# Performance work log

Measured on AMD Instinct MI355X. Metric: run time of the kernel, lower is better.

Reference implementation:

```python
import jax, jax.numpy as jnp
import numpy as np

N = 200000   # active voxels
C = 128      # in_channels == out_channels -> identity downsample
K = 27       # 3x3x3 kernel offsets
EPS = 1e-5


def setup_inputs() -> dict:
    key = jax.random.key(0)
    ks = jax.random.split(key, 4)
    x = jax.random.normal(ks[0], (N, C), jnp.float32)
    nbr = jax.random.randint(ks[1], (N, K), 0, N, jnp.int32)
    W1 = jax.random.normal(ks[2], (K, C, C), jnp.float32) * 0.05
    W2 = jax.random.normal(ks[3], (K, C, C), jnp.float32) * 0.05
    g1 = jnp.ones((C,), jnp.float32); b1 = jnp.zeros((C,), jnp.float32)
    g2 = jnp.ones((C,), jnp.float32); b2 = jnp.zeros((C,), jnp.float32)
    return {"x": x, "nbr": nbr, "W1": W1, "g1": g1, "b1": b1,
            "W2": W2, "g2": g2, "b2": b2}


def _sparse_conv(x, nbr, W):
    # gather-matmul-scatter sparse conv: out[i] = sum_k W[k]^T x[nbr[i,k]]
    # scan over the K=27 kernel offsets to avoid materializing [N,K,C].
    def body(acc, kn):
        Wk, nk = kn                               # [C,C], [N]
        return acc + jnp.take(x, nk, axis=0) @ Wk, None
    acc0 = jnp.zeros((x.shape[0], W.shape[2]), x.dtype)
    out, _ = jax.lax.scan(body, acc0, (W, nbr.T))
    return out


def _bn(x, g, b):
    # training-mode batch norm over the point dimension
    m = jnp.mean(x, axis=0)
    v = jnp.var(x, axis=0)
    return (x - m) * jax.lax.rsqrt(v + EPS) * g + b


def reference(x, nbr, W1, g1, b1, W2, g2, b2):
    out = jax.nn.relu(_bn(_sparse_conv(x, nbr, W1), g1, b1))
    out = _bn(_sparse_conv(out, nbr, W2), g2, b2)
    # downsample is identity (in_channels == out_channels, stride == 1)
    return jax.nn.relu(out + x)
```

## Files before the change

### kernel.cpp

```cpp
#include <hip/hip_runtime.h>
#include <hip/hip_bf16.h>
#include <stdint.h>

#define C_DIM 128
#define K_DIM 27

typedef __attribute__((ext_vector_type(8))) short short8;
typedef __attribute__((ext_vector_type(4))) float f32x4;
typedef __attribute__((ext_vector_type(4))) unsigned short ushort4v;

#define VMCNT8() asm volatile("s_waitcnt vmcnt(8)" ::: "memory")
#define VMCNT6() asm volatile("s_waitcnt vmcnt(6)" ::: "memory")
#define VMCNT4() asm volatile("s_waitcnt vmcnt(4)" ::: "memory")
#define VMCNT0() asm volatile("s_waitcnt vmcnt(0)" ::: "memory")
#define LGKM0() asm volatile("s_waitcnt lgkmcnt(0)" ::: "memory")
#define BAR() __builtin_amdgcn_s_barrier()

__device__ __forceinline__ unsigned short f2bf(float f) {
  unsigned int u = __builtin_bit_cast(unsigned int, f);
  u += 0x7fffu + ((u >> 16) & 1u);
  return (unsigned short)(u >> 16);
}
__device__ __forceinline__ float bf2f(unsigned short h) {
  unsigned int u = ((unsigned int)h) << 16;
  return __builtin_bit_cast(float, u);
}

__device__ __forceinline__ void async_copy16(const void* gsrc, void* ldst) {
  __builtin_amdgcn_global_load_lds(
      (const __attribute__((address_space(1))) unsigned int*)gsrc,
      (__attribute__((address_space(3))) unsigned int*)ldst, 16, 0, 0);
}

__global__ __launch_bounds__(256) void prep_kernel(
    const float* __restrict__ W1, const float* __restrict__ W2,
    unsigned short* __restrict__ Wt1, unsigned short* __restrict__ Wt2,
    float* __restrict__ stats, int stats_n) {
  int idx = blockIdx.x * 256 + threadIdx.x;
  const int total = K_DIM * C_DIM * C_DIM;
  if (idx < total) {
    int cq = idx & 31;
    int co = (idx >> 5) & 127;
    int q  = (idx >> 12) & 3;
    int k  = idx >> 14;
    int ci = q * 32 + cq;
    int src = (k * C_DIM + ci) * C_DIM + co;
    Wt1[idx] = f2bf(W1[src]);
    Wt2[idx] = f2bf(W2[src]);
  }
  if (idx < stats_n) stats[idx] = 0.f;
}

__global__ __launch_bounds__(256) void cvt_x_kernel(
    const float* __restrict__ x, unsigned short* __restrict__ xb, int total4) {
  int i = blockIdx.x * 256 + threadIdx.x;
  if (i >= total4) return;
  f32x4 v = ((const f32x4*)x)[i];
  ushort4v u;
#pragma unroll
  for (int j = 0; j < 4; ++j) u[j] = f2bf(v[j]);
  ((ushort4v*)xb)[i] = u;
}

template<int OUT_IS_F32>
__global__ __launch_bounds__(256, 3) void conv_kernel(
    const unsigned short* __restrict__ xb, const int* __restrict__ nbr,
    const unsigned short* __restrict__ Wt, void* __restrict__ out_v,
    float* __restrict__ stats, int N) {
  extern __shared__ __align__(16) char smem[];
  unsigned short* Abuf = (unsigned short*)smem;
  int* idx_lds = (int*)(smem + 32768);
  float* s_sum = (float*)(smem + 32768 + 13824);
  float* s_ssum = s_sum + C_DIM;

  const int tid = threadIdx.x;
  const int wave = tid >> 6, lane = tid & 63;
  const int lr = lane & 15, lg = lane >> 4;
  const int rg = wave >> 1, cg = wave & 1;
  const int row0 = blockIdx.x * 128;

  if (tid < C_DIM) { s_sum[tid] = 0.f; s_ssum[tid] = 0.f; }

  for (int i = tid; i < 128 * K_DIM; i += 256) {
    int r = i / K_DIM;
    int k = i - r * K_DIM;
    int rr = row0 + r; if (rr >= N) rr = N - 1;
    idx_lds[i] = nbr[(size_t)rr * K_DIM + k];
  }
  __syncthreads();

  const int srow = lane >> 2;
  const int ssw = ((lane & 3) ^ (srow & 3)) << 3;
  const int gr0 = wave * 32 + srow;
  const int gr1 = gr0 + 16;

  auto stage = [&](int a0i, int a1i, int q, int buf) {
    unsigned short* dst = Abuf + buf * 4096 + wave * 1024;
    async_copy16(xb + (size_t)a0i * C_DIM + q * 32 + ssw, dst);
    async_copy16(xb + (size_t)a1i * C_DIM + q * 32 + ssw, dst + 512);
  };

  const unsigned short* wbase = Wt + (size_t)(cg * 64 + lr) * 32 + lg * 8;
  short8 wE[4], wO[4];
  auto wload = [&](short8 (&w)[4], int p) {
    const unsigned short* wp = wbase + (size_t)p * 4096;
#pragma unroll
    for (int ct = 0; ct < 4; ++ct)
      w[ct] = *(const short8*)(wp + ct * 512);
  };

  f32x4 acc[4][4] = {};
  const unsigned short* abase =
      Abuf + (rg * 64 + lr) * 32 + ((lg ^ (lr & 3)) << 3);

  auto compute = [&](const unsigned short* ab, const short8 (&w)[4]) {
    short8 a[4];
#pragma unroll
    for (int rt = 0; rt < 4; ++rt)
      a[rt] = *(const short8*)(ab + rt * 512);
    __builtin_amdgcn_s_setprio(1);
#pragma unroll
    for (int rt = 0; rt < 4; ++rt)
#pragma unroll
      for (int ct = 0; ct < 4; ++ct)
        acc[rt][ct] = __builtin_amdgcn_mfma_f32_16x16x32_bf16(a[rt], w[ct], acc[rt][ct], 0, 0, 0);
    __builtin_amdgcn_s_setprio(0);
  };

  int gA = idx_lds[gr0 * K_DIM];
  int gB = idx_lds[gr1 * K_DIM];
  stage(gA, gB, 0, 0);
  wload(wE, 0);
  stage(gA, gB, 1, 1);
  stage(gA, gB, 2, 2);
  VMCNT8();
  BAR();

  for (int base = 0; base < 104; base += 4) {
    const int k1 = (base >> 2) + 1;
    int hA, hB;
    wload(wO, base + 1);
    stage(gA, gB, 3, 3);
    hA = idx_lds[gr0 * K_DIM + k1];
    hB = idx_lds[gr1 * K_DIM + k1];
    VMCNT8();
    compute(abase, wE);
    LGKM0(); BAR();
    wload(wE, base + 2);
    stage(hA, hB, 0, 0);
    VMCNT8();
    compute(abase + 4096, wO);
    LGKM0(); BAR();
    wload(wO, base + 3);
    stage(hA, hB, 1, 1);
    VMCNT8();
    compute(abase + 8192, wE);
    LGKM0(); BAR();
    wload(wE, base + 4);
    stage(hA, hB, 2, 2);
    VMCNT8();
    compute(abase + 12288, wO);
    LGKM0(); BAR();
    gA = hA; gB = hB;
  }

  wload(wO, 105);
  stage(gA, gB, 3, 3);
  VMCNT8();
  compute(abase, wE);
  LGKM0(); BAR();
  wload(wE, 106);
  VMCNT6();
  compute(abase + 4096, wO);
  LGKM0(); BAR();
  wload(wO, 107);
  VMCNT4();
  compute(abase + 8192, wE);
  LGKM0(); BAR();
  VMCNT0();
  compute(abase + 12288, wO);

  float ps[4] = {0.f, 0.f, 0.f, 0.f}, pss[4] = {0.f, 0.f, 0.f, 0.f};
#pragma unroll
  for (int rt = 0; rt < 4; ++rt) {
#pragma unroll
    for (int j = 0; j < 4; ++j) {
      int grow = row0 + rg * 64 + rt * 16 + lg * 4 + j;
      bool ok = grow < N;
#pragma unroll
      for (int ct = 0; ct < 4; ++ct) {
        float v = acc[rt][ct][j];
        if (ok) {
          int col = cg * 64 + ct * 16 + lr;
          if (OUT_IS_F32)
            ((float*)out_v)[(size_t)grow * C_DIM + col] = v;
          else
            ((unsigned short*)out_v)[(size_t)grow * C_DIM + col] = f2bf(v);
          ps[ct] += v;
          pss[ct] += v * v;
        }
      }
    }
  }
#pragma unroll
  for (int ct = 0; ct < 4; ++ct) {
    ps[ct]  += __shfl_xor(ps[ct], 16, 64);
    ps[ct]  += __shfl_xor(ps[ct], 32, 64);
    pss[ct] += __shfl_xor(pss[ct], 16, 64);
    pss[ct] += __shfl_xor(pss[ct], 32, 64);
    if (lg == 0) {
      int col = cg * 64 + ct * 16 + lr;
      atomicAdd(&s_sum[col], ps[ct]);
      atomicAdd(&s_ssum[col], pss[ct]);
    }
  }
  __syncthreads();
  if (tid < C_DIM) {
    atomicAdd(&stats[tid], s_sum[tid]);
    atomicAdd(&stats[C_DIM + tid], s_ssum[tid]);
  }
}

__global__ void finalize_kernel(const float* __restrict__ stats,
                                const float* __restrict__ g,
                                const float* __restrict__ b,
                                float* __restrict__ sshift, float invN) {
  int c = threadIdx.x;
  float mean = stats[c] * invN;
  float var = stats[128 + c] * invN - mean * mean;
  float sc = g[c] * rsqrtf(var + 1e-5f);
  sshift[c] = sc;
  sshift[128 + c] = b[c] - mean * sc;
}

__global__ __launch_bounds__(256) void apply_kernel(
    unsigned short* __restrict__ y, const float* __restrict__ ss, int total8) {
  int i = blockIdx.x * 256 + threadIdx.x;
  if (i >= total8) return;
  int cb = (i * 8) & 127;
  short8 u = ((short8*)y)[i];
#pragma unroll
  for (int j = 0; j < 8; ++j) {
    float f = bf2f((unsigned short)u[j]) * ss[cb + j] + ss[128 + cb + j];
    u[j] = (short)f2bf(fmaxf(f, 0.f));
  }
  ((short8*)y)[i] = u;
}

__global__ __launch_bounds__(256) void final_kernel(
    float* __restrict__ y2, const float* __restrict__ x,
    const float* __restrict__ ss, int total4) {
  int i = blockIdx.x * 256 + threadIdx.x;
  if (i >= total4) return;
  int cb = (i * 4) & 127;
  f32x4 v = ((const f32x4*)y2)[i];
  f32x4 xv = ((const f32x4*)x)[i];
#pragma unroll
  for (int j = 0; j < 4; ++j)
    v[j] = fmaxf(v[j] * ss[cb + j] + ss[128 + cb + j] + xv[j], 0.f);
  ((f32x4*)y2)[i] = v;
}

extern "C" void kernel_launch(void* const* d_in, const int* in_sizes, int n_in,
                              void* d_out, int out_size, void* d_ws, size_t ws_size,
                              hipStream_t stream) {
  const float* x  = (const float*)d_in[0];
  const int* nbr  = (const int*)d_in[1];
  const float* W1 = (const float*)d_in[2];
  const float* g1 = (const float*)d_in[3];
  const float* b1 = (const float*)d_in[4];
  const float* W2 = (const float*)d_in[5];
  const float* g2 = (const float*)d_in[6];
  const float* b2 = (const float*)d_in[7];
  float* out = (float*)d_out;

  const int N = in_sizes[0] / C_DIM;
  const int totalW = K_DIM * C_DIM * C_DIM;
  const int SMEM_BYTES = 32768 + 13824 + 1024;

  char* ws = (char*)d_ws;
  size_t off = 0;
  auto alloc = [&](size_t bytes) {
    void* p = ws + off;
    off = (off + bytes + 255) & ~(size_t)255;
    return p;
  };
  unsigned short* Wt1 = (unsigned short*)alloc((size_t)totalW * 2);
  unsigned short* Wt2 = (unsigned short*)alloc((size_t)totalW * 2);
  float* stats = (float*)alloc(512 * 4);
  float* ss1   = (float*)alloc(256 * 4);
  float* ss2   = (float*)alloc(256 * 4);
  unsigned short* y1 = (unsigned short*)alloc((size_t)N * C_DIM * 2);
  unsigned short* xb_ws = (unsigned short*)alloc((size_t)N * C_DIM * 2);
  unsigned short* xb = (off <= ws_size) ? xb_ws : (unsigned short*)d_out;

  const int nblk = (N + 127) / 128;
  const float invN = 1.0f / (float)N;

  prep_kernel<<<(totalW + 255) / 256, 256, 0, stream>>>(W1, W2, Wt1, Wt2, stats, 512);

  {
    int t4 = N * C_DIM / 4;
    cvt_x_kernel<<<(t4 + 255) / 256, 256, 0, stream>>>(x, xb, t4);
  }

  conv_kernel<0><<<nblk, 256, SMEM_BYTES, stream>>>(xb, nbr, Wt1, y1, stats, N);
  finalize_kernel<<<1, 128, 0, stream>>>(stats, g1, b1, ss1, invN);

  {
    int t8 = N * C_DIM / 8;
    apply_kernel<<<(t8 + 255) / 256, 256, 0, stream>>>(y1, ss1, t8);
  }

  conv_kernel<1><<<nblk, 256, SMEM_BYTES, stream>>>(y1, nbr, Wt2, out, stats + 256, N);
  finalize_kernel<<<1, 128, 0, stream>>>(stats + 256, g2, b2, ss2, invN);

  {
    int t4 = N * C_DIM / 4;
    final_kernel<<<(t4 + 255) / 256, 256, 0, stream>>>(out, x, ss2, t4);
  }
}
```

Baseline: 656.4 us.

## Deepen weight prefetch to two stages and change LDS swizzle pattern

Result: no change. 652.0 us (-0.7%).

```diff
diff --git a/kernel.cpp b/kernel.cpp
--- a/kernel.cpp
+++ b/kernel.cpp
@@ -9,10 +9,11 @@
 typedef __attribute__((ext_vector_type(4))) float f32x4;
 typedef __attribute__((ext_vector_type(4))) unsigned short ushort4v;
 
-#define VMCNT8() asm volatile("s_waitcnt vmcnt(8)" ::: "memory")
-#define VMCNT6() asm volatile("s_waitcnt vmcnt(6)" ::: "memory")
-#define VMCNT4() asm volatile("s_waitcnt vmcnt(4)" ::: "memory")
-#define VMCNT0() asm volatile("s_waitcnt vmcnt(0)" ::: "memory")
+#define FENCE() asm volatile("" ::: "memory")
+#define VMCNT12() asm volatile("s_waitcnt vmcnt(12)" ::: "memory")
+#define VMCNT10() asm volatile("s_waitcnt vmcnt(10)" ::: "memory")
+#define VMCNT4()  asm volatile("s_waitcnt vmcnt(4)" ::: "memory")
+#define VMCNT0()  asm volatile("s_waitcnt vmcnt(0)" ::: "memory")
 #define LGKM0() asm volatile("s_waitcnt lgkmcnt(0)" ::: "memory")
 #define BAR() __builtin_amdgcn_s_barrier()
 
@@ -89,9 +90,8 @@
   }
   __syncthreads();
 
-  const int srow = lane >> 2;
-  const int ssw = ((lane & 3) ^ (srow & 3)) << 3;
-  const int gr0 = wave * 32 + srow;
+  const int ssw = ((lane & 3) ^ ((lane >> 3) & 3)) << 3;
+  const int gr0 = wave * 32 + (lane >> 2);
   const int gr1 = gr0 + 16;
 
   auto stage = [&](int a0i, int a1i, int q, int buf) {
@@ -101,84 +101,88 @@
   };
 
   const unsigned short* wbase = Wt + (size_t)(cg * 64 + lr) * 32 + lg * 8;
-  short8 wE[4], wO[4];
-  auto wload = [&](short8 (&w)[4], int p) {
-    const unsigned short* wp = wbase + (size_t)p * 4096;
-#pragma unroll
-    for (int ct = 0; ct < 4; ++ct)
-      w[ct] = *(const short8*)(wp + ct * 512);
-  };
+  short8 w0[4], w1[4], w2[4], w3[4];
+#define WLOAD(W, P)                                                      \
+  do {                                                                   \
+    const unsigned short* wp_ = wbase + (size_t)(P) * 4096;              \
+    _Pragma("unroll")                                                    \
+    for (int ct = 0; ct < 4; ++ct) W[ct] = *(const short8*)(wp_ + ct * 512); \
+  } while (0)
 
   f32x4 acc[4][4] = {};
   const unsigned short* abase =
-      Abuf + (rg * 64 + lr) * 32 + ((lg ^ (lr & 3)) << 3);
-
-  auto compute = [&](const unsigned short* ab, const short8 (&w)[4]) {
-    short8 a[4];
-#pragma unroll
-    for (int rt = 0; rt < 4; ++rt)
-      a[rt] = *(const short8*)(ab + rt * 512);
-    __builtin_amdgcn_s_setprio(1);
-#pragma unroll
-    for (int rt = 0; rt < 4; ++rt)
-#pragma unroll
-      for (int ct = 0; ct < 4; ++ct)
-        acc[rt][ct] = __builtin_amdgcn_mfma_f32_16x16x32_bf16(a[rt], w[ct], acc[rt][ct], 0, 0, 0);
-    __builtin_amdgcn_s_setprio(0);
-  };
+      Abuf + (rg * 64 + lr) * 32 + ((lg ^ ((lr >> 1) & 3)) << 3);
+
+#define COMPUTE(BUFOFS, W)                                               \
+  do {                                                                   \
+    short8 a_[4];                                                        \
+    _Pragma("unroll")                                                    \
+    for (int rt = 0; rt < 4; ++rt)                                       \
+      a_[rt] = *(const short8*)(abase + (BUFOFS) + rt * 512);            \
+    __builtin_amdgcn_s_setprio(1);                                       \
+    _Pragma("unroll")                                                    \
+    for (int rt = 0; rt < 4; ++rt)                                       \
+      _Pragma("unroll")                                                  \
+      for (int ct = 0; ct < 4; ++ct)                                     \
+        acc[rt][ct] = __builtin_amdgcn_mfma_f32_16x16x32_bf16(           \
+            a_[rt], W[ct], acc[rt][ct], 0, 0, 0);                        \
+    __builtin_amdgcn_s_setprio(0);                                       \
+  } while (0)
 
   int gA = idx_lds[gr0 * K_DIM];
   int gB = idx_lds[gr1 * K_DIM];
-  stage(gA, gB, 0, 0);
-  wload(wE, 0);
-  stage(gA, gB, 1, 1);
-  stage(gA, gB, 2, 2);
-  VMCNT8();
+  stage(gA, gB, 0, 0); FENCE();
+  stage(gA, gB, 1, 1); FENCE();
+  WLOAD(w0, 0); FENCE();
+  stage(gA, gB, 2, 2); FENCE();
+  WLOAD(w1, 1); FENCE();
+  VMCNT12();
   BAR();
 
   for (int base = 0; base < 104; base += 4) {
     const int k1 = (base >> 2) + 1;
     int hA, hB;
-    wload(wO, base + 1);
-    stage(gA, gB, 3, 3);
+    stage(gA, gB, 3, 3); FENCE();
+    WLOAD(w2, base + 2); FENCE();
     hA = idx_lds[gr0 * K_DIM + k1];
     hB = idx_lds[gr1 * K_DIM + k1];
-    VMCNT8();
-    compute(abase, wE);
+    VMCNT12();
+    COMPUTE(0, w0);
     LGKM0(); BAR();
-    wload(wE, base + 2);
-    stage(hA, hB, 0, 0);
-    VMCNT8();
-    compute(abase + 4096, wO);
+    stage(hA, hB, 0, 0); FENCE();
+    WLOAD(w3, base + 3); FENCE();
+    VMCNT12();
+    COMPUTE(4096, w1);
     LGKM0(); BAR();
-    wload(wO, base + 3);
-    stage(hA, hB, 1, 1);
-    VMCNT8();
-    compute(abase + 8192, wE);
+    stage(hA, hB, 1, 1); FENCE();
+    WLOAD(w0, base + 4); FENCE();
+    VMCNT12();
+    COMPUTE(8192, w2);
     LGKM0(); BAR();
-    wload(wE, base + 4);
-    stage(hA, hB, 2, 2);
-    VMCNT8();
-    compute(abase + 12288, wO);
+    stage(hA, hB, 2, 2); FENCE();
+    WLOAD(w1, base + 5); FENCE();
+    VMCNT12();
+    COMPUTE(12288, w3);
     LGKM0(); BAR();
     gA = hA; gB = hB;
   }
 
-  wload(wO, 105);
-  stage(gA, gB, 3, 3);
-  VMCNT8();
-  compute(abase, wE);
+  stage(gA, gB, 3, 3); FENCE();
+  WLOAD(w2, 106); FENCE();
+  VMCNT12();
+  COMPUTE(0, w0);
   LGKM0(); BAR();
-  wload(wE, 106);
-  VMCNT6();
-  compute(abase + 4096, wO);
+  WLOAD(w3, 107); FENCE();
+  VMCNT10();
+  COMPUTE(4096, w1);
   LGKM0(); BAR();
-  wload(wO, 107);
   VMCNT4();
-  compute(abase + 8192, wE);
+  COMPUTE(8192, w2);
   LGKM0(); BAR();
   VMCNT0();
-  compute(abase + 12288, wO);
+  COMPUTE(12288, w3);
+#undef WLOAD
+#undef COMPUTE
 
   float ps[4] = {0.f, 0.f, 0.f, 0.f}, pss[4] = {0.f, 0.f, 0.f, 0.f};
 #pragma unroll
```

## Stage weights in LDS, double block rows, transpose neighbor indices

Applied to the files above, without the earlier changes.

New measurement: 600.1 us. 1.09x faster.

```diff
diff --git a/kernel.cpp b/kernel.cpp
--- a/kernel.cpp
+++ b/kernel.cpp
@@ -9,9 +9,8 @@
 typedef __attribute__((ext_vector_type(4))) float f32x4;
 typedef __attribute__((ext_vector_type(4))) unsigned short ushort4v;
 
-#define VMCNT8() asm volatile("s_waitcnt vmcnt(8)" ::: "memory")
-#define VMCNT6() asm volatile("s_waitcnt vmcnt(6)" ::: "memory")
-#define VMCNT4() asm volatile("s_waitcnt vmcnt(4)" ::: "memory")
+#define VMCNT5() asm volatile("s_waitcnt vmcnt(5)" ::: "memory")
+#define VMCNT3() asm volatile("s_waitcnt vmcnt(3)" ::: "memory")
 #define VMCNT0() asm volatile("s_waitcnt vmcnt(0)" ::: "memory")
 #define LGKM0() asm volatile("s_waitcnt lgkmcnt(0)" ::: "memory")
 #define BAR() __builtin_amdgcn_s_barrier()
@@ -39,16 +38,33 @@
   int idx = blockIdx.x * 256 + threadIdx.x;
   const int total = K_DIM * C_DIM * C_DIM;
   if (idx < total) {
-    int cq = idx & 31;
+    int e = idx & 7;
+    int gpos = (idx >> 3) & 3;
     int co = (idx >> 5) & 127;
-    int q  = (idx >> 12) & 3;
-    int k  = idx >> 14;
-    int ci = q * 32 + cq;
+    int p = idx >> 12;
+    int k = p >> 2, q = p & 3;
+    int ci = q * 32 + ((gpos ^ ((co >> 1) & 3)) << 3) + e;
     int src = (k * C_DIM + ci) * C_DIM + co;
     Wt1[idx] = f2bf(W1[src]);
     Wt2[idx] = f2bf(W2[src]);
   }
   if (idx < stats_n) stats[idx] = 0.f;
+}
+
+__global__ __launch_bounds__(256) void tr_kernel(
+    const int* __restrict__ nbr, int* __restrict__ nbrT, int N) {
+  __shared__ int t[64 * K_DIM];
+  const int row0 = blockIdx.x * 64;
+  for (int i = threadIdx.x; i < 64 * K_DIM; i += 256) {
+    int r = i / K_DIM, kk = i - r * K_DIM;
+    int rr = row0 + r;
+    t[kk * 64 + r] = (rr < N) ? nbr[(size_t)rr * K_DIM + kk] : 0;
+  }
+  __syncthreads();
+  for (int j = threadIdx.x; j < K_DIM * 64; j += 256) {
+    int kk = j >> 6, r = j & 63;
+    if (row0 + r < N) nbrT[(size_t)kk * N + row0 + r] = t[j];
+  }
 }
 
 __global__ __launch_bounds__(256) void cvt_x_kernel(
@@ -63,122 +79,107 @@
 }
 
 template<int OUT_IS_F32>
-__global__ __launch_bounds__(256, 3) void conv_kernel(
-    const unsigned short* __restrict__ xb, const int* __restrict__ nbr,
+__global__ __launch_bounds__(512, 4) void conv_kernel(
+    const unsigned short* __restrict__ xb, const int* __restrict__ nbrT,
     const unsigned short* __restrict__ Wt, void* __restrict__ out_v,
     float* __restrict__ stats, int N) {
   extern __shared__ __align__(16) char smem[];
   unsigned short* Abuf = (unsigned short*)smem;
-  int* idx_lds = (int*)(smem + 32768);
-  float* s_sum = (float*)(smem + 32768 + 13824);
+  unsigned short* Wbuf = (unsigned short*)(smem + 49152);
+  float* s_sum = (float*)(smem + 73728);
   float* s_ssum = s_sum + C_DIM;
 
   const int tid = threadIdx.x;
   const int wave = tid >> 6, lane = tid & 63;
   const int lr = lane & 15, lg = lane >> 4;
   const int rg = wave >> 1, cg = wave & 1;
-  const int row0 = blockIdx.x * 128;
+  const int row0 = blockIdx.x * 256;
 
   if (tid < C_DIM) { s_sum[tid] = 0.f; s_ssum[tid] = 0.f; }
 
-  for (int i = tid; i < 128 * K_DIM; i += 256) {
-    int r = i / K_DIM;
-    int k = i - r * K_DIM;
-    int rr = row0 + r; if (rr >= N) rr = N - 1;
-    idx_lds[i] = nbr[(size_t)rr * K_DIM + k];
-  }
-  __syncthreads();
-
   const int srow = lane >> 2;
-  const int ssw = ((lane & 3) ^ (srow & 3)) << 3;
-  const int gr0 = wave * 32 + srow;
-  const int gr1 = gr0 + 16;
-
-  auto stage = [&](int a0i, int a1i, int q, int buf) {
-    unsigned short* dst = Abuf + buf * 4096 + wave * 1024;
-    async_copy16(xb + (size_t)a0i * C_DIM + q * 32 + ssw, dst);
-    async_copy16(xb + (size_t)a1i * C_DIM + q * 32 + ssw, dst + 512);
+  const int ssw = ((lane & 3) ^ ((srow >> 1) & 3)) << 3;
+  int rA = row0 + wave * 32 + srow;      if (rA >= N) rA = N - 1;
+  int rB = row0 + wave * 32 + 16 + srow; if (rB >= N) rB = N - 1;
+
+  auto stage_a = [&](int giA, int giB, int q, int aofs) {
+    unsigned short* dst = Abuf + aofs + wave * 1024;
+    async_copy16(xb + (size_t)giA * C_DIM + q * 32 + ssw, dst);
+    async_copy16(xb + (size_t)giB * C_DIM + q * 32 + ssw, dst + 512);
   };
-
-  const unsigned short* wbase = Wt + (size_t)(cg * 64 + lr) * 32 + lg * 8;
-  short8 wE[4], wO[4];
-  auto wload = [&](short8 (&w)[4], int p) {
-    const unsigned short* wp = wbase + (size_t)p * 4096;
+  auto stage_w = [&](const unsigned short* wsrc, int wofs) {
+    async_copy16(wsrc + wave * 512 + lane * 8, Wbuf + wofs + wave * 512);
+  };
+
+  f32x4 acc[4][4] = {};
+  const int swzr = (lg ^ ((lr >> 1) & 3)) << 3;
+  const int aro = (rg * 64 + lr) * 32 + swzr;
+  const int wro = (cg * 64 + lr) * 32 + swzr;
+
+  auto compute = [&](int cAo, int cWo) {
+    short8 a_[4], b_[4];
+#pragma unroll
+    for (int rt = 0; rt < 4; ++rt)
+      a_[rt] = *(const short8*)(Abuf + cAo + aro + rt * 512);
 #pragma unroll
     for (int ct = 0; ct < 4; ++ct)
-      w[ct] = *(const short8*)(wp + ct * 512);
-  };
-
-  f32x4 acc[4][4] = {};
-  const unsigned short* abase =
-      Abuf + (rg * 64 + lr) * 32 + ((lg ^ (lr & 3)) << 3);
-
-  auto compute = [&](const unsigned short* ab, const short8 (&w)[4]) {
-    short8 a[4];
+      b_[ct] = *(const short8*)(Wbuf + cWo + wro + ct * 512);
+    __builtin_amdgcn_s_setprio(1);
 #pragma unroll
     for (int rt = 0; rt < 4; ++rt)
-      a[rt] = *(const short8*)(ab + rt * 512);
-    __builtin_amdgcn_s_setprio(1);
-#pragma unroll
-    for (int rt = 0; rt < 4; ++rt)
 #pragma unroll
       for (int ct = 0; ct < 4; ++ct)
-        acc[rt][ct] = __builtin_amdgcn_mfma_f32_16x16x32_bf16(a[rt], w[ct], acc[rt][ct], 0, 0, 0);
+        acc[rt][ct] = __builtin_amdgcn_mfma_f32_16x16x32_bf16(
+            a_[rt], b_[ct], acc[rt][ct], 0, 0, 0);
     __builtin_amdgcn_s_setprio(0);
   };
 
-  int gA = idx_lds[gr0 * K_DIM];
-  int gB = idx_lds[gr1 * K_DIM];
-  stage(gA, gB, 0, 0);
-  wload(wE, 0);
-  stage(gA, gB, 1, 1);
-  stage(gA, gB, 2, 2);
-  VMCNT8();
+  int giA = nbrT[rA];
+  int giB = nbrT[rB];
+  stage_a(giA, giB, 0, 0);     stage_w(Wt, 0);
+  stage_a(giA, giB, 1, 8192);  stage_w(Wt + 4096, 4096);
+  VMCNT3();
   BAR();
 
-  for (int base = 0; base < 104; base += 4) {
-    const int k1 = (base >> 2) + 1;
-    int hA, hB;
-    wload(wO, base + 1);
-    stage(gA, gB, 3, 3);
-    hA = idx_lds[gr0 * K_DIM + k1];
-    hB = idx_lds[gr1 * K_DIM + k1];
-    VMCNT8();
-    compute(abase, wE);
-    LGKM0(); BAR();
-    wload(wE, base + 2);
-    stage(hA, hB, 0, 0);
-    VMCNT8();
-    compute(abase + 4096, wO);
-    LGKM0(); BAR();
-    wload(wO, base + 3);
-    stage(hA, hB, 1, 1);
-    VMCNT8();
-    compute(abase + 8192, wE);
-    LGKM0(); BAR();
-    wload(wE, base + 4);
-    stage(hA, hB, 2, 2);
-    VMCNT8();
-    compute(abase + 12288, wO);
-    LGKM0(); BAR();
-    gA = hA; gB = hB;
-  }
-
-  wload(wO, 105);
-  stage(gA, gB, 3, 3);
-  VMCNT8();
-  compute(abase, wE);
-  LGKM0(); BAR();
-  wload(wE, 106);
-  VMCNT6();
-  compute(abase + 4096, wO);
-  LGKM0(); BAR();
-  wload(wO, 107);
-  VMCNT4();
-  compute(abase + 8192, wE);
-  LGKM0(); BAR();
-  VMCNT0();
-  compute(abase + 12288, wO);
+  const unsigned short* wsrc = Wt + 2 * 4096;
+  int cAo = 0, cWo = 0, sAo = 16384, sWo = 8192;
+  int giNA, giNB;
+
+#define ADV() do {                                   \
+    cAo = (cAo == 16384) ? 0 : cAo + 8192;           \
+    sAo = (sAo == 16384) ? 0 : sAo + 8192;           \
+    cWo = (cWo == 8192) ? 0 : cWo + 4096;            \
+    sWo = (sWo == 8192) ? 0 : sWo + 4096;            \
+  } while (0)
+
+  for (int k = 0; k < K_DIM - 1; ++k) {
+    stage_a(giA, giB, 2, sAo); stage_w(wsrc, sWo); wsrc += 4096;
+    giNA = nbrT[(size_t)(k + 1) * N + rA];
+    giNB = nbrT[(size_t)(k + 1) * N + rB];
+    compute(cAo, cWo);
+    VMCNT5(); LGKM0(); BAR(); ADV();
+    stage_a(giA, giB, 3, sAo); stage_w(wsrc, sWo); wsrc += 4096;
+    compute(cAo, cWo);
+    VMCNT5(); LGKM0(); BAR(); ADV();
+    stage_a(giNA, giNB, 0, sAo); stage_w(wsrc, sWo); wsrc += 4096;
+    compute(cAo, cWo);
+    VMCNT3(); LGKM0(); BAR(); ADV();
+    stage_a(giNA, giNB, 1, sAo); stage_w(wsrc, sWo); wsrc += 4096;
+    compute(cAo, cWo);
+    VMCNT3(); LGKM0(); BAR(); ADV();
+    giA = giNA; giB = giNB;
+  }
+
+  stage_a(giA, giB, 2, sAo); stage_w(wsrc, sWo); wsrc += 4096;
+  compute(cAo, cWo);
+  VMCNT3(); LGKM0(); BAR(); ADV();
+  stage_a(giA, giB, 3, sAo); stage_w(wsrc, sWo);
+  compute(cAo, cWo);
+  VMCNT3(); LGKM0(); BAR(); ADV();
+  compute(cAo, cWo);
+  VMCNT0(); LGKM0(); BAR(); ADV();
+  compute(cAo, cWo);
+#undef ADV
 
   float ps[4] = {0.f, 0.f, 0.f, 0.f}, pss[4] = {0.f, 0.f, 0.f, 0.f};
 #pragma unroll
@@ -276,7 +277,7 @@
 
   const int N = in_sizes[0] / C_DIM;
   const int totalW = K_DIM * C_DIM * C_DIM;
-  const int SMEM_BYTES = 32768 + 13824 + 1024;
+  const int SMEM_BYTES = 49152 + 24576 + 1024;
 
   char* ws = (char*)d_ws;
   size_t off = 0;
@@ -290,21 +291,28 @@
   float* stats = (float*)alloc(512 * 4);
   float* ss1   = (float*)alloc(256 * 4);
   float* ss2   = (float*)alloc(256 * 4);
+  int* nbrT    = (int*)alloc((size_t)N * K_DIM * 4);
   unsigned short* y1 = (unsigned short*)alloc((size_t)N * C_DIM * 2);
   unsigned short* xb_ws = (unsigned short*)alloc((size_t)N * C_DIM * 2);
   unsigned short* xb = (off <= ws_size) ? xb_ws : (unsigned short*)d_out;
 
-  const int nblk = (N + 127) / 128;
+  (void)hipFuncSetAttribute((const void*)conv_kernel<0>,
+      hipFuncAttributeMaxDynamicSharedMemorySize, SMEM_BYTES);
+  (void)hipFuncSetAttribute((const void*)conv_kernel<1>,
+      hipFuncAttributeMaxDynamicSharedMemorySize, SMEM_BYTES);
+
+  const int nblk = (N + 255) / 256;
   const float invN = 1.0f / (float)N;
 
   prep_kernel<<<(totalW + 255) / 256, 256, 0, stream>>>(W1, W2, Wt1, Wt2, stats, 512);
+  tr_kernel<<<(N + 63) / 64, 256, 0, stream>>>(nbr, nbrT, N);
 
   {
     int t4 = N * C_DIM / 4;
     cvt_x_kernel<<<(t4 + 255) / 256, 256, 0, stream>>>(x, xb, t4);
   }
 
-  conv_kernel<0><<<nblk, 256, SMEM_BYTES, stream>>>(xb, nbr, Wt1, y1, stats, N);
+  conv_kernel<0><<<nblk, 512, SMEM_BYTES, stream>>>(xb, nbrT, Wt1, y1, stats, N);
   finalize_kernel<<<1, 128, 0, stream>>>(stats, g1, b1, ss1, invN);
 
   {
@@ -312,7 +320,7 @@
     apply_kernel<<<(t8 + 255) / 256, 256, 0, stream>>>(y1, ss1, t8);
   }
 
-  conv_kernel<1><<<nblk, 256, SMEM_BYTES, stream>>>(y1, nbr, Wt2, out, stats + 256, N);
+  conv_kernel<1><<<nblk, 512, SMEM_BYTES, stream>>>(y1, nbrT, Wt2, out, stats + 256, N);
   finalize_kernel<<<1, 128, 0, stream>>>(stats + 256, g2, b2, ss2, invN);
 
   {
```
